# Kernel optimization log

Hardware: AMD Instinct MI355X
Metric: run time of the kernel (lower is better)

Reference implementation:

```python
import jax, jax.numpy as jnp
import numpy as np

B, L, DM = 4, 2048, 1024  # batch, seq len (== l_max, global kernel), d_model; head_dim = 1


def setup_inputs() -> dict:
    key = jax.random.key(0)
    ks = jax.random.split(key, 13)
    n = lambda k, shape, s=1.0: jax.random.normal(k, shape, dtype=jnp.float32) * s
    W_SCALE = 0.02   # keeps activations well-conditioned through the chained convs
    K_SCALE = 0.02
    return {
        "u": n(ks[0], (B, L, DM)),
        "Wq": n(ks[1], (DM, DM), W_SCALE), "bq": n(ks[2], (DM,), W_SCALE),
        "Wk": n(ks[3], (DM, DM), W_SCALE), "bk": n(ks[4], (DM,), W_SCALE),
        "Wv": n(ks[5], (DM, DM), W_SCALE), "bv": n(ks[6], (DM,), W_SCALE),
        "k_kernel": n(ks[7], (DM, L), K_SCALE),
        "k_D": n(ks[8], (DM,)),
        "ssm_kernel": n(ks[9], (DM, L), K_SCALE),
        "D": n(ks[10], (DM,)),
        "Wo": n(ks[11], (DM, DM), W_SCALE), "bo": n(ks[12], (DM,), W_SCALE),
    }


def reference(u, Wq, bq, Wk, bk, Wv, bv, k_kernel, k_D, ssm_kernel, D, Wo, bo):
    # u: (B, L, H) with H = d_model (head_dim = 1)
    Lseq = u.shape[1]
    fft_size = 2 * Lseq  # zero-pad to 2L for linear (causal) convolution

    # q/k/v projections -> (B, H, L)
    q = jnp.einsum('blh,dh->bdl', u, Wq) + bq[None, :, None]
    k = jnp.einsum('blh,dh->bdl', u, Wk) + bk[None, :, None]
    v = jnp.einsum('blh,dh->bdl', u, Wv) + bv[None, :, None]

    # shift conv on k: k <- k_kernel * k (causal FFT conv) + k_D * k
    k_kernel_f = jnp.fft.rfft(k_kernel, n=fft_size)           # (H, F)
    k_f = jnp.fft.rfft(k, n=fft_size)                          # (B, H, F)
    shift_k = jnp.fft.irfft(k_kernel_f[None] * k_f, n=fft_size)[..., :Lseq]
    k = shift_k + k_D[None, :, None] * k

    # head_dim == 1: kv outer product collapses to elementwise gate
    kv = k * v                                                 # (B, H, L)

    # ssm conv on kv (torch's 1/fft_size + norm='forward' irfft == standard irfft)
    kv_f = jnp.fft.rfft(kv, n=fft_size)                        # (B, H, F)
    ssm_kernel_f = jnp.fft.rfft(ssm_kernel, n=fft_size)        # (H, F)
    y = jnp.fft.irfft(kv_f * ssm_kernel_f[None], n=fft_size)[..., :Lseq]
    y = y + kv * D[None, :, None]                              # D skip

    # q gating, then output projection
    y = y * q                                                  # (B, H, L)
    y = jnp.swapaxes(y, 1, 2)                                  # (B, L, H)
    return jnp.einsum('blh,oh->blo', y, Wo) + bo
```

## Files before the change

### kernel.cpp

```cpp
#include <hip/hip_runtime.h>
#include <hip/hip_bf16.h>
#include <stdint.h>

#define DM   1024
#define LSEQ 2048
#define NB   4

typedef __attribute__((ext_vector_type(8))) short  short8;
typedef __attribute__((ext_vector_type(4))) float  floatx4;

__device__ __forceinline__ ushort f2b(float x) {
    union { float f; uint32_t u; } v; v.f = x;
    uint32_t b = v.u + 0x7FFF + ((v.u >> 16) & 1);
    return (ushort)(b >> 16);
}
__device__ __forceinline__ float b2f(ushort x) {
    union { uint32_t u; float f; } v; v.u = ((uint32_t)x) << 16;
    return v.f;
}

__global__ __launch_bounds__(256) void cvt_all_kernel(const float* __restrict__ u,
                                                      const float* __restrict__ Wq,
                                                      const float* __restrict__ Wk,
                                                      const float* __restrict__ Wv,
                                                      const float* __restrict__ Wo,
                                                      ushort* __restrict__ U16,
                                                      ushort* __restrict__ Wcat) {
    const int nu  = NB * LSEQ * DM / 8;
    const int per = DM * DM / 8;
    int i = blockIdx.x * 256 + threadIdx.x;
    const float* src; ushort* dst; int j;
    if (i < nu) { src = u; dst = U16; j = i; }
    else {
        int k = i - nu;
        int r = k / per;
        src = (r == 0) ? Wq : (r == 1) ? Wk : (r == 2) ? Wv : Wo;
        dst = Wcat + (size_t)r * (DM * DM);
        j = k - r * per;
    }
    const float4* p = (const float4*)src + (size_t)j * 2;
    float4 a = p[0], b = p[1];
    union { ushort us[8]; uint4 v; } o;
    o.us[0] = f2b(a.x); o.us[1] = f2b(a.y); o.us[2] = f2b(a.z); o.us[3] = f2b(a.w);
    o.us[4] = f2b(b.x); o.us[5] = f2b(b.y); o.us[6] = f2b(b.z); o.us[7] = f2b(b.w);
    *(uint4*)(dst + (size_t)j * 8) = o.v;
}

template <int MODE>
__global__ __launch_bounds__(512, 2) void gemm_8p(const ushort* __restrict__ Aw,
                                                  const ushort* __restrict__ Bw,
                                                  const float* __restrict__ b0,
                                                  const float* __restrict__ b1,
                                                  const float* __restrict__ b2,
                                                  void* __restrict__ C0v,
                                                  void* __restrict__ C1v,
                                                  void* __restrict__ C2v,
                                                  int N, int nbx) {
    constexpr int K = 1024, BK = 64, NT = K / BK;
    __shared__ char lds[131072];

    const int tid   = threadIdx.x;
    const int wave  = tid >> 6;
    const int lane  = tid & 63;
    const int qlane = lane & 15;
    const int qk    = lane >> 4;
    const int z7    = qlane & 7;
    const int wm    = wave >> 2;
    const int wn    = wave & 3;

    int flat = blockIdx.y * nbx + blockIdx.x;
    int nwg  = nbx * gridDim.y;
    int swz  = (flat & 7) * (nwg >> 3) + (flat >> 3);
    const int tn = (swz % nbx) * 256;
    const int tm = (swz / nbx) * 256;

    const int srcChunkOff   = (((lane & 7) ^ (lane >> 3)) * 8);
    const int srcRowInSlice = (lane >> 3);

#define STAGE_H(TT, ISB, H)                                                                   \
    {                                                                                         \
        const ushort* gbase = (ISB) ? Bw : Aw;                                                \
        const int trow = ((ISB) ? tn : tm) + (H) * 128 + wave * 16 + srcRowInSlice;           \
        char* dst = lds + ((ISB) ? 65536 : 0) + ((((TT) & 1) * 2 + (H)) * 16384) + wave * 2048; \
        const int k0_ = (TT) * BK;                                                            \
        _Pragma("unroll")                                                                     \
        for (int j = 0; j < 2; ++j) {                                                         \
            const ushort* src = gbase + (size_t)(trow + j * 8) * K + k0_ + srcChunkOff;       \
            __builtin_amdgcn_global_load_lds(                                                 \
                (const __attribute__((address_space(1))) void*)src,                           \
                (__attribute__((address_space(3))) void*)(dst + j * 1024), 16, 0, 0);         \
        }                                                                                     \
    }

    short8 af[4][2], af2[4][2], bf0[2][2], bf1[2][2];
    floatx4 acc[2][2][4][2] = {};

#define LDA(TT, MH, AF)                                                                       \
    {                                                                                         \
        const char* Ab = lds + ((((TT) & 1) * 2 + (MH)) * 16384);                             \
        _Pragma("unroll")                                                                     \
        for (int i = 0; i < 4; ++i) {                                                         \
            int lr = wm * 64 + i * 16 + qlane;                                                \
            _Pragma("unroll")                                                                 \
            for (int ks = 0; ks < 2; ++ks)                                                    \
                AF[i][ks] = *(const short8*)(Ab + lr * 128 + (((ks * 4 + qk) ^ z7) << 4));    \
        }                                                                                     \
    }
#define LDB(TT, NH, BF)                                                                       \
    {                                                                                         \
        const char* Bb = lds + 65536 + ((((TT) & 1) * 2 + (NH)) * 16384);                     \
        _Pragma("unroll")                                                                     \
        for (int j = 0; j < 2; ++j) {                                                         \
            int lr = wn * 32 + j * 16 + qlane;                                                \
            _Pragma("unroll")                                                                 \
            for (int ks = 0; ks < 2; ++ks)                                                    \
                BF[j][ks] = *(const short8*)(Bb + lr * 128 + (((ks * 4 + qk) ^ z7) << 4));    \
        }                                                                                     \
    }
#define MFMAQ(MH, NH, AF, BF)                                                                 \
    __builtin_amdgcn_s_setprio(1);                                                           \
    _Pragma("unroll")                                                                         \
    for (int ks = 0; ks < 2; ++ks)                                                            \
        _Pragma("unroll")                                                                     \
        for (int i = 0; i < 4; ++i)                                                           \
            _Pragma("unroll")                                                                 \
            for (int j = 0; j < 2; ++j)                                                       \
                acc[MH][NH][i][j] = __builtin_amdgcn_mfma_f32_16x16x32_bf16(                  \
                    AF[i][ks], BF[j][ks], acc[MH][NH][i][j], 0, 0, 0);                        \
    __builtin_amdgcn_s_setprio(0);
#define BARX  __builtin_amdgcn_s_barrier(); __builtin_amdgcn_sched_barrier(0)

    STAGE_H(0, 0, 0); STAGE_H(0, 1, 0); STAGE_H(0, 1, 1); STAGE_H(0, 0, 1);
    STAGE_H(1, 0, 0); STAGE_H(1, 1, 0); STAGE_H(1, 1, 1);
    asm volatile("s_waitcnt vmcnt(6)" ::: "memory");
    BARX;
    LDA(0, 0, af); LDB(0, 0, bf0);

    for (int t = 0; t < NT; ++t) {
        if (t + 1 < NT) STAGE_H(t + 1, 0, 1);
        LDB(t, 1, bf1);
        MFMAQ(0, 0, af, bf0);
        BARX;
        if (t + 2 < NT) STAGE_H(t + 2, 0, 0);
        LDA(t, 1, af2);
        MFMAQ(0, 1, af, bf1);
        BARX;
        if (t + 2 < NT) STAGE_H(t + 2, 1, 0);
        MFMAQ(1, 0, af2, bf0);
        BARX;
        if (t + 2 < NT) STAGE_H(t + 2, 1, 1);
        if (t + 2 < NT)      { asm volatile("s_waitcnt vmcnt(6)" ::: "memory"); }
        else if (t + 1 < NT) { asm volatile("s_waitcnt vmcnt(0)" ::: "memory"); }
        BARX;
        if (t + 1 < NT) { LDA(t + 1, 0, af); LDB(t + 1, 0, bf0); }
        MFMAQ(1, 1, af2, bf1);
    }
#undef STAGE_H
#undef LDA
#undef LDB
#undef MFMAQ
#undef BARX

#pragma unroll
    for (int mh = 0; mh < 2; ++mh)
#pragma unroll
    for (int nh = 0; nh < 2; ++nh)
#pragma unroll
    for (int i = 0; i < 4; ++i)
#pragma unroll
    for (int j = 0; j < 2; ++j) {
        int n  = tn + nh * 128 + wn * 32 + j * 16 + qlane;
        int m0 = tm + mh * 128 + wm * 64 + i * 16 + qk * 4;
        if (MODE == 0) {
            int proj = n >> 10, dd = n & (DM - 1);
            const float* bb = (proj == 0) ? b0 : (proj == 1) ? b1 : b2;
            ushort* Cb      = (ushort*)((proj == 0) ? C0v : (proj == 1) ? C1v : C2v);
            float bv = bb[dd];
            int b = m0 >> 11, l = m0 & (LSEQ - 1);
            ushort4 val;
            val.x = f2b(acc[mh][nh][i][j][0] + bv);
            val.y = f2b(acc[mh][nh][i][j][1] + bv);
            val.z = f2b(acc[mh][nh][i][j][2] + bv);
            val.w = f2b(acc[mh][nh][i][j][3] + bv);
            *(ushort4*)(Cb + ((size_t)b * DM + dd) * LSEQ + l) = val;
        } else {
            float* C0 = (float*)C0v;
            float bv = b0[n];
#pragma unroll
            for (int r = 0; r < 4; ++r)
                C0[(size_t)(m0 + r) * N + n] = acc[mh][nh][i][j][r] + bv;
        }
    }
}

template <int MODE>
__global__ __launch_bounds__(512, 2) void gemm_bt2(const ushort* __restrict__ Aw,
                                                   const ushort* __restrict__ Bw,
                                                   const float* __restrict__ b0,
                                                   const float* __restrict__ b1,
                                                   const float* __restrict__ b2,
                                                   void* __restrict__ C0v,
                                                   void* __restrict__ C1v,
                                                   void* __restrict__ C2v,
                                                   int M, int N, int K, int nbx) {
    constexpr int BM = 128, BN = 256, BK = 64;
    constexpr int BUFB = 49152;
    __shared__ char lds[3 * BUFB];

    const int tid   = threadIdx.x;
    const int wave  = tid >> 6;
    const int lane  = tid & 63;
    const int qlane = lane & 15;
    const int qk    = lane >> 4;

    int flat = blockIdx.y * nbx + blockIdx.x;
    int nwg  = nbx * gridDim.y;
    int swz  = (flat & 7) * (nwg >> 3) + (flat >> 3);
    const int tn = (swz % nbx) * BN;
    const int tm = (swz / nbx) * BM;

    const int wmo = (wave >> 2) * 64;
    const int wno = (wave & 3) * 64;
    const int NT  = K / BK;

#define STAGE(kt, p)                                                                          \
    {                                                                                         \
        const int k0_ = (kt) * BK;                                                            \
        char* Ab_ = lds + (p) * BUFB;                                                         \
        char* Bb_ = Ab_ + 16384;                                                              \
        _Pragma("unroll")                                                                     \
        for (int j = 0; j < 2; ++j) {                                                         \
            int id = wave * 64 + lane + j * 512;                                              \
            int row = id >> 3, s = id & 7;                                                    \
            const ushort* src = Aw + (size_t)(tm + row) * K + k0_ + ((s ^ (row & 7)) * 8);    \
            __builtin_amdgcn_global_load_lds((const __attribute__((address_space(1))) void*)src, \
                (__attribute__((address_space(3))) void*)(Ab_ + wave * 1024 + j * 8192), 16, 0, 0); \
        }                                                                                     \
        _Pragma("unroll")                                                                     \
        for (int j = 0; j < 4; ++j) {                                                         \
            int id = wave * 64 + lane + j * 512;                                              \
            int row = id >> 3, s = id & 7;                                                    \
            const ushort* src = Bw + (size_t)(tn + row) * K + k0_ + ((s ^ (row & 7)) * 8);    \
            __builtin_amdgcn_global_load_lds((const __attribute__((address_space(1))) void*)src, \
                (__attribute__((address_space(3))) void*)(Bb_ + wave * 1024 + j * 8192), 16, 0, 0); \
        }                                                                                     \
    }

    floatx4 acc[4][4] = {};

    STAGE(0, 0);
    STAGE(1, 1);

    const int z7 = qlane & 7;

    for (int t = 0; t < NT; ++t) {
        const int cur = t % 3;
        if (t < NT - 1) asm volatile("s_waitcnt vmcnt(6)" ::: "memory");
        else            asm volatile("s_waitcnt vmcnt(0)" ::: "memory");
        __builtin_amdgcn_s_barrier();
        __builtin_amdgcn_sched_barrier(0);

        if (t + 2 < NT) STAGE(t + 2, (t + 2) % 3);

        const char* Ab = lds + cur * BUFB;
        const char* Bb = Ab + 16384;
#pragma unroll
        for (int kk = 0; kk < 2; ++kk) {
            const int slot = ((kk * 4 + qk) ^ z7) << 4;
            short8 af[4], bfv[4];
#pragma unroll
            for (int i = 0; i < 4; ++i) {
                int r = wmo + i * 16 + qlane;
                af[i] = *(const short8*)(Ab + r * 128 + slot);
            }
#pragma unroll
            for (int j = 0; j < 4; ++j) {
                int r = wno + j * 16 + qlane;
                bfv[j] = *(const short8*)(Bb + r * 128 + slot);
            }
            __builtin_amdgcn_s_setprio(1);
#pragma unroll
            for (int i = 0; i < 4; ++i)
#pragma unroll
                for (int j = 0; j < 4; ++j)
                    acc[i][j] = __builtin_amdgcn_mfma_f32_16x16x32_bf16(af[i], bfv[j], acc[i][j], 0, 0, 0);
            __builtin_amdgcn_s_setprio(0);
        }
    }
#undef STAGE

#pragma unroll
    for (int i = 0; i < 4; ++i) {
#pragma unroll
        for (int j = 0; j < 4; ++j) {
            int n  = tn + wno + j * 16 + qlane;
            int m0 = tm + wmo + i * 16 + qk * 4;
            if (MODE == 0) {
                int proj = n >> 10, dd = n & (DM - 1);
                const float* bb = (proj == 0) ? b0 : (proj == 1) ? b1 : b2;
                ushort* Cb      = (ushort*)((proj == 0) ? C0v : (proj == 1) ? C1v : C2v);
                float bv = bb[dd];
                int b = m0 >> 11, l = m0 & (LSEQ - 1);
                ushort4 val;
                val.x = f2b(acc[i][j][0] + bv);
                val.y = f2b(acc[i][j][1] + bv);
                val.z = f2b(acc[i][j][2] + bv);
                val.w = f2b(acc[i][j][3] + bv);
                *(ushort4*)(Cb + ((size_t)b * DM + dd) * LSEQ + l) = val;
            } else {
                float* C0 = (float*)C0v;
                float bv = b0[n];
#pragma unroll
                for (int r = 0; r < 4; ++r)
                    C0[(size_t)(m0 + r) * N + n] = acc[i][j][r] + bv;
            }
        }
    }
}

#define KSTR 2096
#define XSTR 2248

__global__ __launch_bounds__(512) void conv_mfma_kernel(const ushort* __restrict__ x,
                                                        const float* __restrict__ ker,
                                                        const float* __restrict__ scale,
                                                        const ushort* __restrict__ gate,
                                                        ushort* __restrict__ out) {
    __shared__ ushort krev[KSTR];
    __shared__ ushort xs[4 * XSTR];
    const int d    = blockIdx.x;
    const int tid  = threadIdx.x;
    const int wave = tid >> 6;
    const int lane = tid & 63;

    {
        int b = wave >> 1, half = wave & 1;
        const ushort* src = x + ((size_t)b * DM + d) * LSEQ + half * 1024 + lane * 8;
        char* dst = (char*)xs + b * (XSTR * 2) + 256 + half * 2048;
#pragma unroll
        for (int c = 0; c < 2; ++c)
            __builtin_amdgcn_global_load_lds((const __attribute__((address_space(1))) void*)(src + c * 512),
                                             (__attribute__((address_space(3))) void*)(dst + c * 1024),
                                             16, 0, 0);
    }
    {
        const float* krow = ker + (size_t)d * LSEQ;
        int e0 = tid * 4;
        float4 kv = *(const float4*)(krow + e0);
        ushort4 o;
        o.x = f2b(kv.w); o.y = f2b(kv.z); o.z = f2b(kv.y); o.w = f2b(kv.x);
        *(ushort4*)(krev + (2060 - e0)) = o;
        uint4 z = {0, 0, 0, 0};
        if (tid < 2)  *(uint4*)((char*)krev + tid * 16) = z;
        if (tid >= 2 && tid < 6) *(uint4*)((char*)krev + 4128 + (tid - 2) * 16) = z;
        if (tid >= 64 && tid < 128) {
            int b = (tid - 64) >> 4, c = (tid - 64) & 15;
            *(uint4*)((char*)xs + b * (XSTR * 2) + c * 16) = z;
        }
        if (tid >= 128 && tid < 144) {
            int b = (tid - 128) >> 2, c = (tid - 128) & 3;
            *(uint4*)((char*)xs + b * (XSTR * 2) + 4352 + c * 16) = z;
        }
    }
    __syncthreads();

    const int qn = lane & 15;
    const int qk = lane >> 4;

    int g[2] = {wave, 15 - wave};
    const int smax_all = 128 * (15 - wave) + 128;

    const int lbase = (qn & 3) * XSTR + 128 + 16 * (qn >> 2) + 8 * qk;

    floatx4 acc[2][2] = {};

    short8 fE[2], fO[2];
#pragma unroll
    for (int gi = 0; gi < 2; ++gi) {
        fE[gi] = *(const short8*)(xs + lbase + 128 * g[gi] + 64);
        fO[gi] = *(const short8*)(xs + lbase + 128 * g[gi] + 32);
    }

#define CSTEP(SS, FP)                                                                        \
    {                                                                                        \
        int b_el = 2063 - qn + 8 * qk - (SS);                                                \
        int A0 = b_el & ~3;                                                                  \
        uint2 w0 = *(const uint2*)(krev + A0);                                               \
        uint2 w1 = *(const uint2*)(krev + A0 + 4);                                           \
        uint2 w2 = *(const uint2*)(krev + A0 + 8);                                           \
        int qsel = (b_el >> 1) & 1;                                                          \
        uint sh  = (uint)(b_el & 1) * 16u;                                                   \
        uint e0 = qsel ? w0.y : w0.x;                                                        \
        uint e1 = qsel ? w1.x : w0.y;                                                        \
        uint e2 = qsel ? w1.y : w1.x;                                                        \
        uint e3 = qsel ? w2.x : w1.y;                                                        \
        uint e4 = qsel ? w2.y : w2.x;                                                        \
        union { uint u[4]; short8 v; } Af;                                                   \
        Af.u[0] = __builtin_amdgcn_alignbit(e1, e0, sh);                                     \
        Af.u[1] = __builtin_amdgcn_alignbit(e2, e1, sh);                                     \
        Af.u[2] = __builtin_amdgcn_alignbit(e3, e2, sh);                                     \
        Af.u[3] = __builtin_amdgcn_alignbit(e4, e3, sh);                                     \
        _Pragma("unroll")                                                                    \
        for (int gi = 0; gi < 2; ++gi) {                                                     \
            if ((SS) <= 128 * g[gi] + 128) {                                                 \
                short8 fN = *(const short8*)(xs + lbase + 128 * g[gi] - (SS));               \
                acc[gi][0] = __builtin_amdgcn_mfma_f32_16x16x32_bf16(Af.v, fN, acc[gi][0], 0, 0, 0); \
                acc[gi][1] = __builtin_amdgcn_mfma_f32_16x16x32_bf16(Af.v, FP[gi], acc[gi][1], 0, 0, 0); \
                FP[gi] = fN;                                                                 \
            }                                                                                \
        }                                                                                    \
    }

    for (int s = 0; s <= smax_all; s += 64) {
        CSTEP(s, fE);
        if (s + 32 <= smax_all) CSTEP(s + 32, fO);
    }
#undef CSTEP

    const float sc = scale[d];
#pragma unroll
    for (int gi = 0; gi < 2; ++gi) {
#pragma unroll
        for (int m = 0; m < 2; ++m) {
            int p  = 8 * g[gi] + 4 * m + (qn >> 2);
            int b  = qn & 3;
            int l0 = 16 * p + 4 * qk;
            size_t off = ((size_t)b * DM + d) * LSEQ + l0;
            ushort4 xv = *(const ushort4*)(xs + b * XSTR + 128 + l0);
            ushort4 gv = *(const ushort4*)(gate + off);
            ushort4 ov;
            ov.x = f2b((acc[gi][m][0] + sc * b2f(xv.x)) * b2f(gv.x));
            ov.y = f2b((acc[gi][m][1] + sc * b2f(xv.y)) * b2f(gv.y));
            ov.z = f2b((acc[gi][m][2] + sc * b2f(xv.z)) * b2f(gv.z));
            ov.w = f2b((acc[gi][m][3] + sc * b2f(xv.w)) * b2f(gv.w));
            *(ushort4*)(out + off) = ov;
        }
    }
}

__global__ __launch_bounds__(256) void transpose_bf16(const ushort* __restrict__ in,
                                                      ushort* __restrict__ out) {
    __shared__ ushort t[32][36];
    const int l0 = blockIdx.x * 32;
    const int d0 = blockIdx.y * 32;
    const int b  = blockIdx.z;
    const int q  = threadIdx.x & 7;
    const int r  = threadIdx.x >> 3;
    *(ushort4*)(&t[r][q * 4]) = *(const ushort4*)(in + ((size_t)b * DM + d0 + r) * LSEQ + l0 + q * 4);
    __syncthreads();
    ushort4 o;
    o.x = t[q * 4 + 0][r]; o.y = t[q * 4 + 1][r]; o.z = t[q * 4 + 2][r]; o.w = t[q * 4 + 3][r];
    *(ushort4*)(out + ((size_t)b * LSEQ + l0 + r) * DM + d0 + q * 4) = o;
}

extern "C" void kernel_launch(void* const* d_in, const int* in_sizes, int n_in,
                              void* d_out, int out_size, void* d_ws, size_t ws_size,
                              hipStream_t stream) {
    const float* u        = (const float*)d_in[0];
    const float* Wq       = (const float*)d_in[1];
    const float* bq       = (const float*)d_in[2];
    const float* Wk       = (const float*)d_in[3];
    const float* bk       = (const float*)d_in[4];
    const float* Wv       = (const float*)d_in[5];
    const float* bv       = (const float*)d_in[6];
    const float* k_kernel = (const float*)d_in[7];
    const float* k_D      = (const float*)d_in[8];
    const float* ssm_ker  = (const float*)d_in[9];
    const float* Dv       = (const float*)d_in[10];
    const float* Wo       = (const float*)d_in[11];
    const float* bo       = (const float*)d_in[12];
    float* outp = (float*)d_out;

    char* ws = (char*)d_ws;
    ushort* Q    = (ushort*)(ws);
    ushort* KV   = (ushort*)(ws + (16ull << 20));
    ushort* V    = (ushort*)(ws + (32ull << 20));
    ushort* U16  = (ushort*)(ws + (48ull << 20));
    ushort* YT   = (ushort*)(ws + (64ull << 20));
    ushort* Wcat = (ushort*)(ws + (80ull << 20));

    const int nu = NB * LSEQ * DM / 8, nw = 4 * DM * DM / 8;
    cvt_all_kernel<<<(nu + nw) / 256, 256, 0, stream>>>(u, Wq, Wk, Wv, Wo, U16, Wcat);

    dim3 g1(3 * DM / 256, NB * LSEQ / 256);
    gemm_8p<0><<<g1, 512, 0, stream>>>(U16, Wcat, bq, bk, bv, Q, KV, V,
                                       3 * DM, 3 * DM / 256);

    conv_mfma_kernel<<<DM, 512, 0, stream>>>(KV, k_kernel, k_D, V, KV);
    conv_mfma_kernel<<<DM, 512, 0, stream>>>(KV, ssm_ker, Dv, Q, KV);

    dim3 g2(LSEQ / 32, DM / 32, NB);
    transpose_bf16<<<g2, 256, 0, stream>>>(KV, YT);

    dim3 g3(DM / 256, NB * LSEQ / 128);
    gemm_bt2<1><<<g3, 512, 0, stream>>>(YT, Wcat + 3 * DM * DM, bo, bo, bo,
                                        outp, outp, outp, NB * LSEQ, DM, DM, DM / 256);
}
```

Measured before the change: 166.4 us.

## Fuse shift conv and SSM conv into one kernel keeping kv in LDS

After: 162.6 us. -2.3%, faster.

```diff
diff --git a/kernel.cpp b/kernel.cpp
--- a/kernel.cpp
+++ b/kernel.cpp
@@ -321,12 +321,16 @@
 #define KSTR 2096
 #define XSTR 2248
 
-__global__ __launch_bounds__(512) void conv_mfma_kernel(const ushort* __restrict__ x,
-                                                        const float* __restrict__ ker,
-                                                        const float* __restrict__ scale,
-                                                        const ushort* __restrict__ gate,
-                                                        ushort* __restrict__ out) {
-    __shared__ ushort krev[KSTR];
+__global__ __launch_bounds__(512) void conv_fused_kernel(const ushort* __restrict__ x,
+                                                         const float* __restrict__ ker1,
+                                                         const float* __restrict__ scale1,
+                                                         const ushort* __restrict__ gate1,
+                                                         const float* __restrict__ ker2,
+                                                         const float* __restrict__ scale2,
+                                                         const ushort* __restrict__ gate2,
+                                                         ushort* __restrict__ out) {
+    __shared__ ushort krev1[KSTR];
+    __shared__ ushort krev2[KSTR];
     __shared__ ushort xs[4 * XSTR];
     const int d    = blockIdx.x;
     const int tid  = threadIdx.x;
@@ -344,15 +348,23 @@
                                              16, 0, 0);
     }
     {
-        const float* krow = ker + (size_t)d * LSEQ;
         int e0 = tid * 4;
-        float4 kv = *(const float4*)(krow + e0);
-        ushort4 o;
-        o.x = f2b(kv.w); o.y = f2b(kv.z); o.z = f2b(kv.y); o.w = f2b(kv.x);
-        *(ushort4*)(krev + (2060 - e0)) = o;
+        float4 k1 = *(const float4*)(ker1 + (size_t)d * LSEQ + e0);
+        float4 k2 = *(const float4*)(ker2 + (size_t)d * LSEQ + e0);
+        ushort4 o1, o2;
+        o1.x = f2b(k1.w); o1.y = f2b(k1.z); o1.z = f2b(k1.y); o1.w = f2b(k1.x);
+        o2.x = f2b(k2.w); o2.y = f2b(k2.z); o2.z = f2b(k2.y); o2.w = f2b(k2.x);
+        *(ushort4*)(krev1 + (2060 - e0)) = o1;
+        *(ushort4*)(krev2 + (2060 - e0)) = o2;
         uint4 z = {0, 0, 0, 0};
-        if (tid < 2)  *(uint4*)((char*)krev + tid * 16) = z;
-        if (tid >= 2 && tid < 6) *(uint4*)((char*)krev + 4128 + (tid - 2) * 16) = z;
+        if (tid < 2) {
+            *(uint4*)((char*)krev1 + tid * 16) = z;
+            *(uint4*)((char*)krev2 + tid * 16) = z;
+        }
+        if (tid >= 2 && tid < 6) {
+            *(uint4*)((char*)krev1 + 4128 + (tid - 2) * 16) = z;
+            *(uint4*)((char*)krev2 + 4128 + (tid - 2) * 16) = z;
+        }
         if (tid >= 64 && tid < 128) {
             int b = (tid - 64) >> 4, c = (tid - 64) & 15;
             *(uint4*)((char*)xs + b * (XSTR * 2) + c * 16) = z;
@@ -372,22 +384,13 @@
 
     const int lbase = (qn & 3) * XSTR + 128 + 16 * (qn >> 2) + 8 * qk;
 
-    floatx4 acc[2][2] = {};
-
-    short8 fE[2], fO[2];
-#pragma unroll
-    for (int gi = 0; gi < 2; ++gi) {
-        fE[gi] = *(const short8*)(xs + lbase + 128 * g[gi] + 64);
-        fO[gi] = *(const short8*)(xs + lbase + 128 * g[gi] + 32);
-    }
-
-#define CSTEP(SS, FP)                                                                        \
+#define CSTEP(KR, ACC, SS, FP)                                                               \
     {                                                                                        \
         int b_el = 2063 - qn + 8 * qk - (SS);                                                \
         int A0 = b_el & ~3;                                                                  \
-        uint2 w0 = *(const uint2*)(krev + A0);                                               \
-        uint2 w1 = *(const uint2*)(krev + A0 + 4);                                           \
-        uint2 w2 = *(const uint2*)(krev + A0 + 8);                                           \
+        uint2 w0 = *(const uint2*)((KR) + A0);                                               \
+        uint2 w1 = *(const uint2*)((KR) + A0 + 4);                                           \
+        uint2 w2 = *(const uint2*)((KR) + A0 + 8);                                           \
         int qsel = (b_el >> 1) & 1;                                                          \
         uint sh  = (uint)(b_el & 1) * 16u;                                                   \
         uint e0 = qsel ? w0.y : w0.x;                                                        \
@@ -404,38 +407,83 @@
         for (int gi = 0; gi < 2; ++gi) {                                                     \
             if ((SS) <= 128 * g[gi] + 128) {                                                 \
                 short8 fN = *(const short8*)(xs + lbase + 128 * g[gi] - (SS));               \
-                acc[gi][0] = __builtin_amdgcn_mfma_f32_16x16x32_bf16(Af.v, fN, acc[gi][0], 0, 0, 0); \
-                acc[gi][1] = __builtin_amdgcn_mfma_f32_16x16x32_bf16(Af.v, FP[gi], acc[gi][1], 0, 0, 0); \
+                ACC[gi][0] = __builtin_amdgcn_mfma_f32_16x16x32_bf16(Af.v, fN, ACC[gi][0], 0, 0, 0); \
+                ACC[gi][1] = __builtin_amdgcn_mfma_f32_16x16x32_bf16(Af.v, FP[gi], ACC[gi][1], 0, 0, 0); \
                 FP[gi] = fN;                                                                 \
             }                                                                                \
         }                                                                                    \
     }
 
-    for (int s = 0; s <= smax_all; s += 64) {
-        CSTEP(s, fE);
-        if (s + 32 <= smax_all) CSTEP(s + 32, fO);
+    {
+        floatx4 acc[2][2] = {};
+        short8 fE[2], fO[2];
+#pragma unroll
+        for (int gi = 0; gi < 2; ++gi) {
+            fE[gi] = *(const short8*)(xs + lbase + 128 * g[gi] + 64);
+            fO[gi] = *(const short8*)(xs + lbase + 128 * g[gi] + 32);
+        }
+        for (int s = 0; s <= smax_all; s += 64) {
+            CSTEP(krev1, acc, s, fE);
+            if (s + 32 <= smax_all) CSTEP(krev1, acc, s + 32, fO);
+        }
+
+        __syncthreads();
+        const float sc = scale1[d];
+#pragma unroll
+        for (int gi = 0; gi < 2; ++gi) {
+#pragma unroll
+            for (int m = 0; m < 2; ++m) {
+                int p  = 8 * g[gi] + 4 * m + (qn >> 2);
+                int b  = qn & 3;
+                int l0 = 16 * p + 4 * qk;
+                size_t off = ((size_t)b * DM + d) * LSEQ + l0;
+                ushort4 xv = *(const ushort4*)(xs + b * XSTR + 128 + l0);
+                ushort4 gv = *(const ushort4*)(gate1 + off);
+                ushort4 ov;
+                ov.x = f2b((acc[gi][m][0] + sc * b2f(xv.x)) * b2f(gv.x));
+                ov.y = f2b((acc[gi][m][1] + sc * b2f(xv.y)) * b2f(gv.y));
+                ov.z = f2b((acc[gi][m][2] + sc * b2f(xv.z)) * b2f(gv.z));
+                ov.w = f2b((acc[gi][m][3] + sc * b2f(xv.w)) * b2f(gv.w));
+                *(ushort4*)(xs + b * XSTR + 128 + l0) = ov;
+            }
+        }
+        __syncthreads();
+    }
+
+    {
+        floatx4 acc[2][2] = {};
+        short8 fE[2], fO[2];
+#pragma unroll
+        for (int gi = 0; gi < 2; ++gi) {
+            fE[gi] = *(const short8*)(xs + lbase + 128 * g[gi] + 64);
+            fO[gi] = *(const short8*)(xs + lbase + 128 * g[gi] + 32);
+        }
+        for (int s = 0; s <= smax_all; s += 64) {
+            CSTEP(krev2, acc, s, fE);
+            if (s + 32 <= smax_all) CSTEP(krev2, acc, s + 32, fO);
+        }
+
+        const float sc = scale2[d];
+#pragma unroll
+        for (int gi = 0; gi < 2; ++gi) {
+#pragma unroll
+            for (int m = 0; m < 2; ++m) {
+                int p  = 8 * g[gi] + 4 * m + (qn >> 2);
+                int b  = qn & 3;
+                int l0 = 16 * p + 4 * qk;
+                size_t off = ((size_t)b * DM + d) * LSEQ + l0;
+                ushort4 xv = *(const ushort4*)(xs + b * XSTR + 128 + l0);
+                ushort4 gv = *(const ushort4*)(gate2 + off);
+                ushort4 ov;
+                ov.x = f2b((acc[gi][m][0] + sc * b2f(xv.x)) * b2f(gv.x));
+                ov.y = f2b((acc[gi][m][1] + sc * b2f(xv.y)) * b2f(gv.y));
+                ov.z = f2b((acc[gi][m][2] + sc * b2f(xv.z)) * b2f(gv.z));
+                ov.w = f2b((acc[gi][m][3] + sc * b2f(xv.w)) * b2f(gv.w));
+                *(ushort4*)(out + off) = ov;
+            }
+        }
     }
 #undef CSTEP
-
-    const float sc = scale[d];
-#pragma unroll
-    for (int gi = 0; gi < 2; ++gi) {
-#pragma unroll
-        for (int m = 0; m < 2; ++m) {
-            int p  = 8 * g[gi] + 4 * m + (qn >> 2);
-            int b  = qn & 3;
-            int l0 = 16 * p + 4 * qk;
-            size_t off = ((size_t)b * DM + d) * LSEQ + l0;
-            ushort4 xv = *(const ushort4*)(xs + b * XSTR + 128 + l0);
-            ushort4 gv = *(const ushort4*)(gate + off);
-            ushort4 ov;
-            ov.x = f2b((acc[gi][m][0] + sc * b2f(xv.x)) * b2f(gv.x));
-            ov.y = f2b((acc[gi][m][1] + sc * b2f(xv.y)) * b2f(gv.y));
-            ov.z = f2b((acc[gi][m][2] + sc * b2f(xv.z)) * b2f(gv.z));
-            ov.w = f2b((acc[gi][m][3] + sc * b2f(xv.w)) * b2f(gv.w));
-            *(ushort4*)(out + off) = ov;
-        }
-    }
 }
 
 __global__ __launch_bounds__(256) void transpose_bf16(const ushort* __restrict__ in,
@@ -486,8 +534,7 @@
     gemm_8p<0><<<g1, 512, 0, stream>>>(U16, Wcat, bq, bk, bv, Q, KV, V,
                                        3 * DM, 3 * DM / 256);
 
-    conv_mfma_kernel<<<DM, 512, 0, stream>>>(KV, k_kernel, k_D, V, KV);
-    conv_mfma_kernel<<<DM, 512, 0, stream>>>(KV, ssm_ker, Dv, Q, KV);
+    conv_fused_kernel<<<DM, 512, 0, stream>>>(KV, k_kernel, k_D, V, ssm_ker, Dv, Q, KV);
 
     dim3 g2(LSEQ / 32, DM / 32, NB);
     transpose_bf16<<<g2, 256, 0, stream>>>(KV, YT);
```
